# Optimization experiments

Measured on AMD Instinct MI355X. Metric: run time of the kernel, lower is better.

## Reference

```python
import jax, jax.numpy as jnp
import numpy as np

B, H, D = 2048, 50, 400          # batch, history_length, news/category embed dim
S, C = 285, 18                   # num_subcategories, num_categories
NC = 50                          # num_clicks_embed_dim (= history_length table size)
FILL = 1e-30                     # masked_fill value used by the original module


def setup_inputs() -> dict:
    key = jax.random.key(0)
    ks = jax.random.split(key, 9)
    vectors = jax.random.normal(ks[0], (B, H, D), dtype=jnp.float32)
    subcategory = jax.random.randint(ks[1], (B, H), 0, S, dtype=jnp.int32)
    category = jax.random.randint(ks[2], (B, H), 0, C, dtype=jnp.int32)
    subcat_embed = jax.random.normal(ks[3], (S, D), dtype=jnp.float32) * 0.02
    cat_embed = jax.random.normal(ks[4], (C, D), dtype=jnp.float32) * 0.02
    clicks_embed = jax.random.normal(ks[5], (H, NC), dtype=jnp.float32) * 0.02
    w_news = jax.random.normal(ks[6], (D,), dtype=jnp.float32) * 0.05
    w_subcat = jax.random.normal(ks[7], (D + NC,), dtype=jnp.float32) * 0.05
    w_cat = jax.random.normal(ks[8], (D + NC,), dtype=jnp.float32) * 0.05
    return {"vectors": vectors, "subcategory": subcategory, "category": category,
            "subcat_embed": subcat_embed, "cat_embed": cat_embed,
            "clicks_embed": clicks_embed, "w_news": w_news,
            "w_subcat": w_subcat, "w_cat": w_cat}


def reference(vectors, subcategory, category, subcat_embed, cat_embed,
              clicks_embed, w_news, w_subcat, w_cat):
    sub_mask = jax.nn.one_hot(subcategory, S, dtype=vectors.dtype)   # [B,H,S]
    cat_mask = jax.nn.one_hot(category, C, dtype=vectors.dtype)      # [B,H,C]
    sub_to_cat = jnp.einsum('bhs,bhc->bsc', sub_mask, cat_mask)      # [B,S,C]

    # --- news -> subcategory attention pooling ---
    news_scores = jnp.einsum('bhd,d->bh', vectors, w_news)           # [B,H]
    scores = jnp.where(sub_mask > 0, news_scores[:, :, None], FILL)  # [B,H,S]
    news_w = jax.nn.softmax(scores, axis=1)
    sub_news_repr = jnp.einsum('bhs,bhd->bsd', news_w, vectors)      # [B,S,D]
    sub_repr = sub_news_repr + subcat_embed[None]                    # [B,S,D]

    sub_clicks = sub_mask.sum(axis=1)                                # [B,S] float counts
    sub_weights = sub_clicks / sub_clicks.sum(axis=1, keepdims=True)
    sub_clicks_emb = clicks_embed[sub_clicks.astype(jnp.int32)]      # [B,S,NC]

    # --- subcategory -> category attention pooling ---
    sc_scores = jnp.einsum('bsk,k->bs',
                           jnp.concatenate([sub_repr, sub_clicks_emb], axis=2),
                           w_subcat)                                 # [B,S]
    scores2 = jnp.where(sub_to_cat > 0, sc_scores[:, :, None], FILL) # [B,S,C]
    sub_w = jax.nn.softmax(scores2, axis=1)
    cat_sub_repr = jnp.einsum('bsc,bsd->bcd', sub_w, sub_repr)       # [B,C,D]
    cat_repr = cat_sub_repr + cat_embed[None]                        # [B,C,D]

    cat_clicks = cat_mask.sum(axis=1)                                # [B,C]
    cat_weights = cat_clicks / cat_clicks.sum(axis=1, keepdims=True)
    cat_clicks_emb = clicks_embed[cat_clicks.astype(jnp.int32)]      # [B,C,NC]

    # --- category -> user attention pooling (unmasked) ---
    c_scores = jnp.einsum('bck,k->bc',
                          jnp.concatenate([cat_repr, cat_clicks_emb], axis=2),
                          w_cat)                                     # [B,C]
    cat_w = jax.nn.softmax(c_scores, axis=1)
    user_repr = jnp.einsum('bc,bcd->bd', cat_w, cat_repr)            # [B,D]

    return (sub_repr, sub_weights, cat_repr, cat_weights, user_repr)
```

## Files before the change

### kernel.cpp

```cpp
#include <hip/hip_runtime.h>

#define BB 2048
#define HH 50
#define DD 400
#define D4 100
#define SS 285
#define CC 18
#define NCC 50
#define FILLV 1e-30f

static constexpr int BLOCK = 256;

static constexpr size_t OFF1 = (size_t)BB * SS * DD;
static constexpr size_t OFF2 = OFF1 + (size_t)BB * SS;
static constexpr size_t OFF3 = OFF2 + (size_t)BB * CC * DD;
static constexpr size_t OFF4 = OFF3 + (size_t)BB * CC;

#define WS_ETOT 0
#define WS_SCE  400
#define WS_SEW  688
#define WS_CEDS 976
#define WS_CEDC 1026
#define WS_CEW  1076
#define WS_BATCH 1152
#define PB_BASE  0
#define PB_LIST  400
#define PB_NU    685
#define PB_STRIDE 688
static constexpr size_t NEEDED_WS_BYTES =
    (size_t)(WS_BATCH + (size_t)BB * PB_STRIDE) * 4;

typedef float f4 __attribute__((ext_vector_type(4)));
typedef unsigned long long u64;

__device__ __forceinline__ float dot4(f4 a, f4 b) {
    return a.x * b.x + a.y * b.y + a.z * b.z + a.w * b.w;
}

__global__ void hierec_pre(const float* __restrict__ subcat_embed,
                           const float* __restrict__ cat_embed,
                           const float* __restrict__ clicks_embed,
                           const float* __restrict__ w_subcat,
                           const float* __restrict__ w_cat,
                           float* __restrict__ ws)
{
    const int tid  = threadIdx.x;
    const int lane = tid & 63;
    const int wave = tid >> 6;
    const int wpb  = blockDim.x >> 6;
    const int gw   = blockIdx.x * wpb + wave;
    const int nw   = gridDim.x * wpb;

    for (int s = gw; s < SS; s += nw) {
        float p1 = 0.f, p2 = 0.f;
        for (int d = lane; d < DD; d += 64) {
            float v = subcat_embed[s * DD + d];
            p1 += v * w_subcat[d];
            p2 += v * w_cat[d];
        }
        for (int off = 32; off; off >>= 1) {
            p1 += __shfl_down(p1, off);
            p2 += __shfl_down(p2, off);
        }
        if (lane == 0) { ws[WS_SCE + s] = p1; ws[WS_SEW + s] = p2; }
    }
    if (blockIdx.x == 0) {
        for (int d = tid; d < DD; d += blockDim.x) {
            float a = 0.f;
            for (int s = 0; s < SS; ++s) a += subcat_embed[s * DD + d];
            ws[WS_ETOT + d] = a;
        }
    }
    if (blockIdx.x == 1) {
        for (int k = wave; k < HH; k += wpb) {
            float p1 = 0.f, p2 = 0.f;
            if (lane < NCC) {
                float v = clicks_embed[k * NCC + lane];
                p1 = v * w_subcat[DD + lane];
                p2 = v * w_cat[DD + lane];
            }
            for (int off = 32; off; off >>= 1) {
                p1 += __shfl_down(p1, off);
                p2 += __shfl_down(p2, off);
            }
            if (lane == 0) { ws[WS_CEDS + k] = p1; ws[WS_CEDC + k] = p2; }
        }
    }
    if (blockIdx.x == 2) {
        for (int c = wave; c < CC; c += wpb) {
            float p = 0.f;
            for (int d = lane; d < DD; d += 64) p += cat_embed[c * DD + d] * w_cat[d];
            for (int off = 32; off; off >>= 1) p += __shfl_down(p, off);
            if (lane == 0) ws[WS_CEW + c] = p;
        }
    }
}

__global__ __launch_bounds__(BLOCK, 8) void hierec_main(
    const float* __restrict__ vectors,
    const int*   __restrict__ subcategory,
    const int*   __restrict__ category,
    const float* __restrict__ subcat_embed,
    const float* __restrict__ cat_embed,
    const float* __restrict__ w_news,
    const float* __restrict__ w_subcat,
    const float* __restrict__ w_cat,
    float* __restrict__ ws,
    float* __restrict__ out,
    int split)
{
    const int b    = blockIdx.x;
    const int tid  = threadIdx.x;
    const int lane = tid & 63;
    const int wave = tid >> 6;
    const float* pre = ws;

    __shared__ f4     vt4L[D4];
    __shared__ f4     et4L[D4];
    __shared__ f4     Wt4L[D4];
    __shared__ float  coefS[SS];
    __shared__ u64    maskS[SS];
    __shared__ int    cntS[SS];
    __shared__ float  ns1L[HH], ns2L[HH], ns3L[HH];
    __shared__ float  uzL[HH], wNL[HH], scL[HH], Wn3sL[HH];
    __shared__ u64    maskL[HH];
    __shared__ int    hsL[HH], hcL[HH], repL[HH], prepL[HH];
    __shared__ float  mcL[CC], ucL[CC], rZcL[CC], csL[CC], catwL[CC];
    __shared__ int    cntcL[CC];
    __shared__ int    prepStart[CC + 1];
    __shared__ int    prepSL[HH];
    __shared__ float  prepGL[HH];
    __shared__ int    clickedL[HH];
    __shared__ int    unclkL[SS];
    __shared__ int    npL, ndL, nUcnt;
    __shared__ float  PvL, vtwL, etwL, Wn3totL;

    const float* vb  = vectors + (size_t)b * HH * DD;
    const f4*    vb4 = (const f4*)vb;
    const f4*    se4 = (const f4*)subcat_embed;
    const f4*    ce4 = (const f4*)cat_embed;
    f4* o4 = (f4*)(out + (size_t)b * SS * DD);

    if (tid < HH) {
        hsL[tid] = subcategory[b * HH + tid];
        hcL[tid] = category[b * HH + tid];
    }
    for (int s = tid; s < SS; s += BLOCK) {
        coefS[s] = 1.f / (float)HH;
        maskS[s] = 0ull;
        cntS[s]  = 0;
    }
    if (tid < D4) {
        et4L[tid] = ((const f4*)pre)[tid];
        f4 z = {0.f, 0.f, 0.f, 0.f};
        vt4L[tid] = z;
        Wt4L[tid] = z;
    }
    if (tid == 0) nUcnt = 0;
    __syncthreads();

    {
        const f4* wn4 = (const f4*)w_news;
        const f4* ws4 = (const f4*)w_subcat;
        const f4* wc4 = (const f4*)w_cat;
        const bool hi = lane < (D4 - 64);
        f4 vtp0 = {0.f, 0.f, 0.f, 0.f};
        f4 vtp1 = {0.f, 0.f, 0.f, 0.f};
        for (int h = wave; h < HH; h += 4) {
            f4 v0 = vb4[h * D4 + lane];
            float p1 = dot4(v0, wn4[lane]);
            float p2 = dot4(v0, ws4[lane]);
            float p3 = dot4(v0, wc4[lane]);
            vtp0 += v0;
            if (hi) {
                f4 v1 = vb4[h * D4 + 64 + lane];
                p1 += dot4(v1, wn4[64 + lane]);
                p2 += dot4(v1, ws4[64 + lane]);
                p3 += dot4(v1, wc4[64 + lane]);
                vtp1 += v1;
            }
            for (int off = 32; off; off >>= 1) {
                p1 += __shfl_down(p1, off);
                p2 += __shfl_down(p2, off);
                p3 += __shfl_down(p3, off);
            }
            if (lane == 0) { ns1L[h] = p1; ns2L[h] = p2; ns3L[h] = p3; }
        }
        float* vtf = (float*)vt4L;
        atomicAdd(&vtf[4 * lane + 0], vtp0.x);
        atomicAdd(&vtf[4 * lane + 1], vtp0.y);
        atomicAdd(&vtf[4 * lane + 2], vtp0.z);
        atomicAdd(&vtf[4 * lane + 3], vtp0.w);
        if (hi) {
            atomicAdd(&vtf[4 * (64 + lane) + 0], vtp1.x);
            atomicAdd(&vtf[4 * (64 + lane) + 1], vtp1.y);
            atomicAdd(&vtf[4 * (64 + lane) + 2], vtp1.z);
            atomicAdd(&vtf[4 * (64 + lane) + 3], vtp1.w);
        }
    }
    __syncthreads();

    if (tid < HH) {
        const int h = tid;
        const int s = hsL[h], c = hcL[h];
        u64 mask = 0ull, pmask = 0ull;
        for (int j = 0; j < HH; ++j) {
            bool ms = (hsL[j] == s);
            mask  |= (u64)(ms ? 1 : 0) << j;
            pmask |= (u64)((ms && hcL[j] == c) ? 1 : 0) << j;
        }
        int cnt = __popcll(mask);
        bool rep = ((__ffsll((long long)mask) - 1) == h);

        float m = FILLV;
        u64 t = mask;
        while (t) { int j = __ffsll((long long)t) - 1; t &= t - 1; m = fmaxf(m, ns1L[j]); }
        float u = expf(FILLV - m);
        float sumE = 0.f, sum2 = 0.f;
        t = mask;
        while (t) {
            int j = __ffsll((long long)t) - 1; t &= t - 1;
            float e = expf(ns1L[j] - m);
            sumE += e;
            sum2 += (e - u) * ns2L[j];
        }
        float Z = sumE + (float)(HH - cnt) * u;
        float vt2 = 0.f;
        for (int j = 0; j < HH; ++j) vt2 += ns2L[j];
        int ci = cnt < (NCC - 1) ? cnt : (NCC - 1);
        float sc = (sum2 + u * vt2) / Z + pre[WS_SCE + s] + pre[WS_CEDS + ci];

        float e_h = expf(ns1L[h] - m);
        float uz = u / Z;
        wNL[h] = (e_h - u) / Z;
        uzL[h] = uz; maskL[h] = mask; scL[h] = sc;
        repL[h]  = rep ? 1 : 0;
        prepL[h] = ((__ffsll((long long)pmask) - 1) == h) ? 1 : 0;
        if (rep) { coefS[s] = uz; maskS[s] = mask; cntS[s] = cnt; }
    } else if (wave == 1) {
        float p = 0.f;
        const float* et = (const float*)et4L;
        for (int d = lane; d < DD; d += 64) p += et[d] * w_cat[d];
        for (int off = 32; off; off >>= 1) p += __shfl_down(p, off);
        if (lane == 0) etwL = p;
    } else if (wave == 2) {
        float p = (lane < HH) ? ns3L[lane] : 0.f;
        for (int off = 32; off; off >>= 1) p += __shfl_down(p, off);
        if (lane == 0) vtwL = p;
    }
    __syncthreads();

    if (tid < CC) {
        const int c = tid;
        float mc = FILLV; int n = 0, cc2 = 0;
        for (int j = 0; j < HH; ++j) {
            if (hcL[j] == c) ++cc2;
            if (prepL[j] && hcL[j] == c) { ++n; mc = fmaxf(mc, scL[j]); }
        }
        float u = expf(FILLV - mc);
        float sumE = 0.f;
        for (int j = 0; j < HH; ++j)
            if (prepL[j] && hcL[j] == c) sumE += expf(scL[j] - mc);
        float Zc = sumE + (float)(SS - n) * u;
        mcL[c] = mc; ucL[c] = u; rZcL[c] = 1.f / Zc; cntcL[c] = cc2;
        __builtin_nontemporal_store((float)cc2 * (1.f / (float)HH),
                                    &out[OFF3 + (size_t)b * CC + c]);
    } else if (tid == 64) {
        int nd = 0, np = 0;
        float sumUb = 0.f;
        for (int j = 0; j < HH; ++j) {
            if (repL[j]) { clickedL[nd] = hsL[j]; ++nd; sumUb += uzL[j]; }
            if (prepL[j]) ++np;
        }
        npL = np; ndL = nd;
        PvL = (float)(SS - nd) * (1.f / (float)HH) + sumUb;
    } else if (tid >= 128 && tid < 128 + HH) {
        const int h = tid - 128;
        float a = 0.f;
        u64 t = maskL[h];
        while (t) { int j = __ffsll((long long)t) - 1; t &= t - 1; a += wNL[j] * ns3L[j]; }
        Wn3sL[h] = a;
    } else if (wave == 3) {
        const int l = tid - 192;
        float p = (l < HH) ? wNL[l] * ns3L[l] : 0.f;
        for (int off = 32; off; off >>= 1) p += __shfl_down(p, off);
        if (l == 0) Wn3totL = p;
    }
    for (int s = tid; s < SS; s += BLOCK) {
        __builtin_nontemporal_store((float)cntS[s] * (1.f / (float)HH),
                                    &out[OFF1 + (size_t)b * SS + s]);
        if (maskS[s] == 0ull) {
            int p = atomicAdd(&nUcnt, 1);
            unclkL[p] = s;
        }
    }
    __syncthreads();

    if (tid < CC) {
        const int c = tid;
        int start = 0;
        for (int j = 0; j < HH; ++j)
            if (prepL[j] && hcL[j] < c) ++start;
        prepStart[c] = start;
        if (c == 0) prepStart[CC] = npL;
        int cur = start;
        float segs = 0.f;
        for (int j = 0; j < HH; ++j) {
            if (prepL[j] && hcL[j] == c) {
                float g = expf(scL[j] - mcL[c]) - ucL[c];
                prepSL[cur] = hsL[j]; prepGL[cur] = g;
                segs += g * (uzL[j] * vtwL + Wn3sL[j] + pre[WS_SEW + hsL[j]]);
                ++cur;
            }
        }
        int ci = cntcL[c] < (NCC - 1) ? cntcL[c] : (NCC - 1);
        csL[c] = rZcL[c] * (ucL[c] * (PvL * vtwL + etwL + Wn3totL) + segs)
                 + pre[WS_CEW + c] + pre[WS_CEDC + ci];
    }
    __syncthreads();

    if (tid < CC) {
        float m = csL[0];
        for (int j = 1; j < CC; ++j) m = fmaxf(m, csL[j]);
        float Zc = 0.f;
        for (int j = 0; j < CC; ++j) Zc += expf(csL[j] - m);
        catwL[tid] = expf(csL[tid] - m) / Zc;
    }
    __syncthreads();

    {
        const int tot = ndL * D4;
        for (int i = tid; i < tot; i += BLOCK) {
            int ii = i / D4;
            int q  = i - ii * D4;
            int s  = clickedL[ii];
            f4 wsacc = {0.f, 0.f, 0.f, 0.f};
            u64 t = maskS[s];
            while (t) {
                int j = __ffsll((long long)t) - 1; t &= t - 1;
                wsacc += wNL[j] * vb4[j * D4 + q];
            }
            float* wt = (float*)&Wt4L[q];
            atomicAdd(&wt[0], wsacc.x);
            atomicAdd(&wt[1], wsacc.y);
            atomicAdd(&wt[2], wsacc.z);
            atomicAdd(&wt[3], wsacc.w);
            f4 val = coefS[s] * vt4L[q] + wsacc + se4[s * D4 + q];
            o4[s * D4 + q] = val;
        }
    }
    __syncthreads();


    if (tid < D4) {
        const int q = tid;
        f4 SubTot = PvL * vt4L[q] + Wt4L[q] + et4L[q];
        f4 uacc = {0.f, 0.f, 0.f, 0.f};
        f4* oc = (f4*)(out + OFF2 + (size_t)b * CC * DD);
        for (int c = 0; c < CC; ++c) {
            f4 acc = ucL[c] * SubTot;
            const int e = prepStart[c + 1];
            for (int jj = prepStart[c]; jj < e; ++jj)
                acc += prepGL[jj] * o4[prepSL[jj] * D4 + q];
            f4 val = rZcL[c] * acc + ce4[c * D4 + q];
            uacc += catwL[c] * val;
            __builtin_nontemporal_store(val, &oc[c * D4 + q]);
        }
        f4* ou = (f4*)(out + OFF4 + (size_t)b * DD);
        __builtin_nontemporal_store(uacc, &ou[q]);
    }

    if (split) {
        float* wb = ws + WS_BATCH + (size_t)b * PB_STRIDE;
        if (tid < D4) ((f4*)wb)[tid] = (1.f / (float)HH) * vt4L[tid];
        const int nU = nUcnt;
        int* wlist = (int*)(wb + PB_LIST);
        for (int i = tid; i < nU; i += BLOCK) wlist[i] = unclkL[i];
        if (tid == 0) ((int*)(wb + PB_NU))[0] = nU;
    } else {
        const int tot = (SS - ndL) * D4;
        const float cst = 1.f / (float)HH;
        for (int i = tid; i < tot; i += BLOCK) {
            int u = i / D4;
            int q = i - u * D4;
            int s = unclkL[u];
            f4 acc = cst * vt4L[q] + se4[s * D4 + q];
            __builtin_nontemporal_store(acc, &o4[s * D4 + q]);
        }
    }
}

static constexpr int CHUNKS = 4;

__global__ __launch_bounds__(BLOCK, 8) void hierec_stream(
    const float* __restrict__ subcat_embed,
    const float* __restrict__ ws,
    float* __restrict__ out)
{
    const int b   = blockIdx.x / CHUNKS;
    const int ch  = blockIdx.x % CHUNKS;
    const int tid = threadIdx.x;

    __shared__ f4  baseL[D4];
    __shared__ int listL[(SS + CHUNKS - 1) / CHUNKS + 1];

    const float* wb = ws + WS_BATCH + (size_t)b * PB_STRIDE;
    if (tid < D4) baseL[tid] = ((const f4*)wb)[tid];

    const int nU  = ((const int*)(wb + PB_NU))[0];
    const int per = (nU + CHUNKS - 1) / CHUNKS;
    int r0 = ch * per; if (r0 > nU) r0 = nU;
    int r1 = r0 + per; if (r1 > nU) r1 = nU;
    const int nrows = r1 - r0;

    const int* list = (const int*)(wb + PB_LIST);
    for (int i = tid; i < nrows; i += BLOCK) listL[i] = list[r0 + i];
    __syncthreads();

    const f4* se4 = (const f4*)subcat_embed;
    f4* o4 = (f4*)(out + (size_t)b * SS * DD);
    const int items = nrows * D4;
    for (int i = tid; i < items; i += BLOCK) {
        int u = i / D4;
        int q = i - u * D4;
        int s = listL[u];
        f4 v = baseL[q] + se4[s * D4 + q];
        __builtin_nontemporal_store(v, &o4[s * D4 + q]);
    }
}

extern "C" void kernel_launch(void* const* d_in, const int* in_sizes, int n_in,
                              void* d_out, int out_size, void* d_ws, size_t ws_size,
                              hipStream_t stream) {
    const float* vectors      = (const float*)d_in[0];
    const int*   subcategory  = (const int*)d_in[1];
    const int*   category     = (const int*)d_in[2];
    const float* subcat_embed = (const float*)d_in[3];
    const float* cat_embed    = (const float*)d_in[4];
    const float* clicks_embed = (const float*)d_in[5];
    const float* w_news       = (const float*)d_in[6];
    const float* w_subcat     = (const float*)d_in[7];
    const float* w_cat        = (const float*)d_in[8];
    float* out = (float*)d_out;
    float* ws  = (float*)d_ws;

    const int split = (ws_size >= NEEDED_WS_BYTES) ? 1 : 0;

    hipLaunchKernelGGL(hierec_pre, dim3(32), dim3(256), 0, stream,
                       subcat_embed, cat_embed, clicks_embed, w_subcat, w_cat, ws);
    hipLaunchKernelGGL(hierec_main, dim3(BB), dim3(BLOCK), 0, stream,
                       vectors, subcategory, category, subcat_embed, cat_embed,
                       w_news, w_subcat, w_cat, ws, out, split);
    if (split) {
        hipLaunchKernelGGL(hierec_stream, dim3(BB * CHUNKS), dim3(BLOCK), 0, stream,
                           subcat_embed, ws, out);
    }
}
```

Before: 512.1 us.

## Retile unclicked-subcategory fill kernel by subcategory tile with bitmask per batch

The streaming kernel that writes rows for unclicked subcategories is reorganised. Previously it used a per-batch index list split across 4 chunks. Now each block owns a tile of 9 subcategory rows, caches those subcat_embed rows in shared memory, and loops over 32 batches, using a per-batch 285-bit bitmask to skip clicked rows. The goal is to reuse embedding rows across batches and write contiguous output tiles. The cost is reading the bitmask and base row for every batch inside the loop, plus divergent predicated stores.

```diff
diff --git a/kernel.cpp b/kernel.cpp
--- a/kernel.cpp
+++ b/kernel.cpp
@@ -24,9 +24,8 @@
 #define WS_CEW  1076
 #define WS_BATCH 1152
 #define PB_BASE  0
-#define PB_LIST  400
-#define PB_NU    685
-#define PB_STRIDE 688
+#define PB_BM    400
+#define PB_STRIDE 416
 static constexpr size_t NEEDED_WS_BYTES =
     (size_t)(WS_BATCH + (size_t)BB * PB_STRIDE) * 4;
 
@@ -373,10 +372,15 @@
     if (split) {
         float* wb = ws + WS_BATCH + (size_t)b * PB_STRIDE;
         if (tid < D4) ((f4*)wb)[tid] = (1.f / (float)HH) * vt4L[tid];
-        const int nU = nUcnt;
-        int* wlist = (int*)(wb + PB_LIST);
-        for (int i = tid; i < nU; i += BLOCK) wlist[i] = unclkL[i];
-        if (tid == 0) ((int*)(wb + PB_NU))[0] = nU;
+        if (tid >= 128 && tid < 128 + 10) {
+            const int w = tid - 128;
+            unsigned word = 0;
+            for (int k = 0; k < 32; ++k) {
+                int s = w * 32 + k;
+                if (s < SS && cntS[s] > 0) word |= (1u << k);
+            }
+            ((unsigned*)(wb + PB_BM))[w] = word;
+        }
     } else {
         const int tot = (SS - ndL) * D4;
         const float cst = 1.f / (float)HH;
@@ -390,42 +394,46 @@
     }
 }
 
-static constexpr int CHUNKS = 4;
+static constexpr int TILE_S = 9;
+static constexpr int NTILES = (SS + TILE_S - 1) / TILE_S;
+static constexpr int NCHUNK = 64;
+static constexpr int BCHUNK = BB / NCHUNK;
 
 __global__ __launch_bounds__(BLOCK, 8) void hierec_stream(
     const float* __restrict__ subcat_embed,
     const float* __restrict__ ws,
     float* __restrict__ out)
 {
-    const int b   = blockIdx.x / CHUNKS;
-    const int ch  = blockIdx.x % CHUNKS;
-    const int tid = threadIdx.x;
-
-    __shared__ f4  baseL[D4];
-    __shared__ int listL[(SS + CHUNKS - 1) / CHUNKS + 1];
-
-    const float* wb = ws + WS_BATCH + (size_t)b * PB_STRIDE;
-    if (tid < D4) baseL[tid] = ((const f4*)wb)[tid];
-
-    const int nU  = ((const int*)(wb + PB_NU))[0];
-    const int per = (nU + CHUNKS - 1) / CHUNKS;
-    int r0 = ch * per; if (r0 > nU) r0 = nU;
-    int r1 = r0 + per; if (r1 > nU) r1 = nU;
-    const int nrows = r1 - r0;
-
-    const int* list = (const int*)(wb + PB_LIST);
-    for (int i = tid; i < nrows; i += BLOCK) listL[i] = list[r0 + i];
-    __syncthreads();
-
-    const f4* se4 = (const f4*)subcat_embed;
-    f4* o4 = (f4*)(out + (size_t)b * SS * DD);
+    const int tid  = threadIdx.x;
+    const int tile = blockIdx.x >> 6;
+    const int chk  = blockIdx.x & (NCHUNK - 1);
+    const int s0   = tile * TILE_S;
+    const int nrows = (s0 + TILE_S <= SS) ? TILE_S : (SS - s0);
     const int items = nrows * D4;
-    for (int i = tid; i < items; i += BLOCK) {
-        int u = i / D4;
-        int q = i - u * D4;
-        int s = listL[u];
-        f4 v = baseL[q] + se4[s * D4 + q];
-        __builtin_nontemporal_store(v, &o4[s * D4 + q]);
+    const int b0   = chk * BCHUNK;
+
+    __shared__ f4 seL[TILE_S * D4];
+
+    const f4* se4 = (const f4*)subcat_embed + (size_t)s0 * D4;
+    for (int i = tid; i < items; i += BLOCK) seL[i] = se4[i];
+    __syncthreads();
+
+    for (int bl = 0; bl < BCHUNK; ++bl) {
+        const int b = b0 + bl;
+        const float* wb = ws + WS_BATCH + (size_t)b * PB_STRIDE;
+        const f4* bb = (const f4*)wb;
+        const unsigned* bm = (const unsigned*)(wb + PB_BM);
+        f4* ob = (f4*)(out + ((size_t)b * SS + s0) * DD);
+        for (int i = tid; i < items; i += BLOCK) {
+            int r = i / D4;
+            int q = i - r * D4;
+            int s = s0 + r;
+            unsigned w = bm[s >> 5];
+            if (!((w >> (s & 31)) & 1u)) {
+                f4 v = bb[q] + seL[i];
+                __builtin_nontemporal_store(v, &ob[(size_t)r * D4 + q]);
+            }
+        }
     }
 }
 
@@ -452,7 +460,7 @@
                        vectors, subcategory, category, subcat_embed, cat_embed,
                        w_news, w_subcat, w_cat, ws, out, split);
     if (split) {
-        hipLaunchKernelGGL(hierec_stream, dim3(BB * CHUNKS), dim3(BLOCK), 0, stream,
+        hipLaunchKernelGGL(hierec_stream, dim3(NTILES * NCHUNK), dim3(BLOCK), 0, stream,
                            subcat_embed, ws, out);
     }
 }
```

Result: no change. 518.3 us (+1.2%).
